# Kernel optimization log

Hardware: AMD Instinct MI355X
Metric: run time of the kernel (lower is better)

The kernel has to match this reference:

```python
import jax, jax.numpy as jnp
import numpy as np

N_NODES = 50000
N_EDGES = 300000
D_IN = 256
D_HID = 256
N_LAYERS = 3
D_OUT = 32
NUM_GRAPHS = 512


def setup_inputs() -> dict:
    key = jax.random.key(0)
    ks = jax.random.split(key, 10)
    x = jax.random.normal(ks[0], (N_NODES, D_IN), dtype=jnp.float32)
    edge_index = jax.random.randint(ks[1], (2, N_EDGES), 0, N_NODES, dtype=jnp.int64)
    batch = jnp.sort(jax.random.randint(ks[2], (N_NODES,), 0, NUM_GRAPHS, dtype=jnp.int64))
    # GraphConv params: out_i = relu(lin_rel(sum_j x_j) + lin_root(x_i)), bias in lin_rel.
    # in_channels == hidden_channels so all nc layers stack into one tensor.
    s = 1.0 / np.sqrt(D_HID)
    W_rel = jax.random.normal(ks[3], (N_LAYERS, D_HID, D_HID), dtype=jnp.float32) * s
    W_root = jax.random.normal(ks[4], (N_LAYERS, D_HID, D_HID), dtype=jnp.float32) * s
    b_conv = jax.random.normal(ks[5], (N_LAYERS, D_HID), dtype=jnp.float32) * s
    W1 = jax.random.normal(ks[6], (D_HID, 4 * D_HID), dtype=jnp.float32) * s
    b1 = jnp.zeros((4 * D_HID,), dtype=jnp.float32)
    W2 = jax.random.normal(ks[7], (4 * D_HID, D_OUT), dtype=jnp.float32) * (1.0 / np.sqrt(4 * D_HID))
    b2 = jnp.zeros((D_OUT,), dtype=jnp.float32)
    return {"x": x, "edge_index": edge_index, "batch": batch,
            "W_rel": W_rel, "W_root": W_root, "b_conv": b_conv,
            "W1": W1, "b1": b1, "W2": W2, "b2": b2,
            "num_graphs": NUM_GRAPHS}


def reference(x, edge_index, batch, W_rel, W_root, b_conv, W1, b1, W2, b2, num_graphs):
    src, dst = edge_index[0], edge_index[1]
    n = x.shape[0]
    # stacked GraphConv(aggr='add') layers with ReLU
    for i in range(W_rel.shape[0]):
        aggr = jax.ops.segment_sum(x[src], dst, num_segments=n)  # [N, d] gather+scatter-add
        x = jax.nn.relu(aggr @ W_rel[i] + x @ W_root[i] + b_conv[i])
    # global_add_pool over graph ids
    pooled = jax.ops.segment_sum(x, batch, num_segments=num_graphs)  # [G, d]
    h = jax.nn.relu(pooled @ W1 + b1)
    return jax.nn.sigmoid(h @ W2 + b2)
```

## Files before the change

kernel.cpp:

```cpp
#include <hip/hip_runtime.h>
#include <math.h>

#define NNODES 50000
#define MPAD   50048
#define D      256
#define K2     512
#define NEDGES 300000
#define NGRAPH 512
#define NLAYERS 3

#define SCB    256
#define NSCB   ((NNODES + SCB - 1) / SCB)

typedef __bf16 bf16x8 __attribute__((ext_vector_type(8)));
typedef float  f32x4  __attribute__((ext_vector_type(4)));

__device__ __forceinline__ ushort f2bf(float f) {
    unsigned u = __float_as_uint(f);
    unsigned r = (u + 0x7FFFu + ((u >> 16) & 1u)) >> 16;
    return (ushort)r;
}
__device__ __forceinline__ float bf2f(ushort b) {
    return __uint_as_float(((unsigned)b) << 16);
}

__device__ __forceinline__ void stage16(const ushort* g, ushort* l) {
    __builtin_amdgcn_global_load_lds(
        (const __attribute__((address_space(1))) unsigned*)g,
        (__attribute__((address_space(3))) unsigned*)l, 16, 0, 0);
}

__global__ __launch_bounds__(256)
void hist_kernel(const int* __restrict__ dst, int* __restrict__ deg, int nE) {
    int e = blockIdx.x * 256 + threadIdx.x;
    if (e < nE) atomicAdd(&deg[dst[e]], 1);
}

__global__ __launch_bounds__(SCB)
void scan_part_kernel(const int* __restrict__ deg, int* __restrict__ bsum) {
    __shared__ int red[SCB];
    int t = threadIdx.x;
    int i = blockIdx.x * SCB + t;
    red[t] = (i < NNODES) ? deg[i] : 0;
    __syncthreads();
#pragma unroll
    for (int off = SCB / 2; off > 0; off >>= 1) {
        if (t < off) red[t] += red[t + off];
        __syncthreads();
    }
    if (t == 0) bsum[blockIdx.x] = red[0];
}

__global__ __launch_bounds__(256)
void scan_bsum_kernel(const int* __restrict__ bsum, int* __restrict__ boff) {
    __shared__ int p[256];
    int t = threadIdx.x;
    p[t] = (t < NSCB) ? bsum[t] : 0;
    __syncthreads();
    for (int off = 1; off < 256; off <<= 1) {
        int v = (t >= off) ? p[t - off] : 0;
        __syncthreads();
        p[t] += v;
        __syncthreads();
    }
    if (t < NSCB) boff[t] = (t == 0) ? 0 : p[t - 1];
}

__global__ __launch_bounds__(SCB)
void scan_final_kernel(const int* __restrict__ deg, const int* __restrict__ boff,
                       int* __restrict__ row_start, int* __restrict__ cursor) {
    __shared__ int p[SCB];
    int t = threadIdx.x;
    int i = blockIdx.x * SCB + t;
    int v = (i < NNODES) ? deg[i] : 0;
    p[t] = v;
    __syncthreads();
    for (int off = 1; off < SCB; off <<= 1) {
        int u = (t >= off) ? p[t - off] : 0;
        __syncthreads();
        p[t] += u;
        __syncthreads();
    }
    int excl = boff[blockIdx.x] + p[t] - v;
    if (i < NNODES) {
        row_start[i] = excl;
        cursor[i] = excl;
    }
    if (blockIdx.x == 0 && t == 0) row_start[NNODES] = NEDGES;
}

__global__ __launch_bounds__(256)
void fill_kernel(const int* __restrict__ src, const int* __restrict__ dst,
                 int* __restrict__ cursor, int* __restrict__ e_src, int nE) {
    int e = blockIdx.x * 256 + threadIdx.x;
    if (e < nE) {
        int pos = atomicAdd(&cursor[dst[e]], 1);
        e_src[pos] = src[e];
    }
}

__global__ __launch_bounds__(256)
void gstart_kernel(const int* __restrict__ batch, int* __restrict__ gstart) {
    int g = blockIdx.x * 256 + threadIdx.x;
    if (g > NGRAPH) return;
    if (g == NGRAPH) { gstart[g] = NNODES; return; }
    int lo = 0, hi = NNODES;
    while (lo < hi) { int mid = (lo + hi) >> 1; if (batch[mid] < g) lo = mid + 1; else hi = mid; }
    gstart[g] = lo;
}

__global__ __launch_bounds__(256)
void prep_w_kernel(const float* __restrict__ W_rel, const float* __restrict__ W_root,
                   ushort* __restrict__ Wh, ushort* __restrict__ Wl) {
    int i = blockIdx.x * 256 + threadIdx.x;
    if (i >= NLAYERS * D * K2) return;
    int L = i / (D * K2);
    int rem = i % (D * K2);
    int n = rem / K2;
    int k = rem % K2;
    float v = (k < D) ? W_rel[(size_t)L * D * D + (size_t)k * D + n]
                      : W_root[(size_t)L * D * D + (size_t)(k - D) * D + n];
    ushort hi = f2bf(v);
    float  lo = v - bf2f(hi);
    Wh[i] = hi;
    Wl[i] = f2bf(lo);
}

__global__ __launch_bounds__(256)
void cvt_x_kernel(const float* __restrict__ x, ushort* __restrict__ xh,
                  ushort* __restrict__ xl) {
    size_t base = ((size_t)blockIdx.x * 256 + threadIdx.x) * 8;
    if (base >= (size_t)MPAD * D) return;
    ushort h[8], l[8];
    if (base < (size_t)NNODES * D) {
        float4 v0 = *reinterpret_cast<const float4*>(x + base);
        float4 v1 = *reinterpret_cast<const float4*>(x + base + 4);
        float vv[8] = {v0.x, v0.y, v0.z, v0.w, v1.x, v1.y, v1.z, v1.w};
#pragma unroll
        for (int j = 0; j < 8; ++j) {
            h[j] = f2bf(vv[j]);
            l[j] = f2bf(vv[j] - bf2f(h[j]));
        }
    } else {
#pragma unroll
        for (int j = 0; j < 8; ++j) { h[j] = 0; l[j] = 0; }
    }
    *reinterpret_cast<uint4*>(xh + base) = *reinterpret_cast<uint4*>(h);
    *reinterpret_cast<uint4*>(xl + base) = *reinterpret_cast<uint4*>(l);
}

__global__ __launch_bounds__(256)
void gather_hl_kernel(const ushort* __restrict__ ph, const ushort* __restrict__ pl,
                      const int* __restrict__ row_start, const int* __restrict__ e_src,
                      ushort* __restrict__ gh, ushort* __restrict__ gl) {
    int t = threadIdx.x;
    int n = blockIdx.x * 4 + (t >> 6);
    if (n >= NNODES) return;
    int lane = t & 63;
    int beg = row_start[n], end = row_start[n + 1];
    float a0 = 0.f, a1 = 0.f, a2 = 0.f, a3 = 0.f;
    int j = beg;
    for (; j + 4 <= end; j += 4) {
        int s0 = e_src[j], s1 = e_src[j + 1], s2 = e_src[j + 2], s3 = e_src[j + 3];
        ushort4 h0 = *reinterpret_cast<const ushort4*>(ph + (size_t)s0 * D + lane * 4);
        ushort4 l0 = *reinterpret_cast<const ushort4*>(pl + (size_t)s0 * D + lane * 4);
        ushort4 h1 = *reinterpret_cast<const ushort4*>(ph + (size_t)s1 * D + lane * 4);
        ushort4 l1 = *reinterpret_cast<const ushort4*>(pl + (size_t)s1 * D + lane * 4);
        ushort4 h2 = *reinterpret_cast<const ushort4*>(ph + (size_t)s2 * D + lane * 4);
        ushort4 l2 = *reinterpret_cast<const ushort4*>(pl + (size_t)s2 * D + lane * 4);
        ushort4 h3 = *reinterpret_cast<const ushort4*>(ph + (size_t)s3 * D + lane * 4);
        ushort4 l3 = *reinterpret_cast<const ushort4*>(pl + (size_t)s3 * D + lane * 4);
        a0 += (bf2f(h0.x) + bf2f(l0.x)) + (bf2f(h1.x) + bf2f(l1.x)) +
              (bf2f(h2.x) + bf2f(l2.x)) + (bf2f(h3.x) + bf2f(l3.x));
        a1 += (bf2f(h0.y) + bf2f(l0.y)) + (bf2f(h1.y) + bf2f(l1.y)) +
              (bf2f(h2.y) + bf2f(l2.y)) + (bf2f(h3.y) + bf2f(l3.y));
        a2 += (bf2f(h0.z) + bf2f(l0.z)) + (bf2f(h1.z) + bf2f(l1.z)) +
              (bf2f(h2.z) + bf2f(l2.z)) + (bf2f(h3.z) + bf2f(l3.z));
        a3 += (bf2f(h0.w) + bf2f(l0.w)) + (bf2f(h1.w) + bf2f(l1.w)) +
              (bf2f(h2.w) + bf2f(l2.w)) + (bf2f(h3.w) + bf2f(l3.w));
    }
    for (; j < end; ++j) {
        int s = e_src[j];
        ushort4 h = *reinterpret_cast<const ushort4*>(ph + (size_t)s * D + lane * 4);
        ushort4 l = *reinterpret_cast<const ushort4*>(pl + (size_t)s * D + lane * 4);
        a0 += bf2f(h.x) + bf2f(l.x);
        a1 += bf2f(h.y) + bf2f(l.y);
        a2 += bf2f(h.z) + bf2f(l.z);
        a3 += bf2f(h.w) + bf2f(l.w);
    }
    ushort4 oh, ol;
    oh.x = f2bf(a0); ol.x = f2bf(a0 - bf2f(oh.x));
    oh.y = f2bf(a1); ol.y = f2bf(a1 - bf2f(oh.y));
    oh.z = f2bf(a2); ol.z = f2bf(a2 - bf2f(oh.z));
    oh.w = f2bf(a3); ol.w = f2bf(a3 - bf2f(oh.w));
    *reinterpret_cast<ushort4*>(gh + (size_t)n * D + lane * 4) = oh;
    *reinterpret_cast<ushort4*>(gl + (size_t)n * D + lane * 4) = ol;
}

#define GBM 128
#define GBN 128
#define GBK 32

__global__ __launch_bounds__(256)
void gemm_hl_kernel(const ushort* __restrict__ Gh, const ushort* __restrict__ Gl,
                    const ushort* __restrict__ Xh, const ushort* __restrict__ Xl,
                    const ushort* __restrict__ Wh, const ushort* __restrict__ Wl,
                    const float* __restrict__ bias,
                    ushort* __restrict__ outh, ushort* __restrict__ outl) {
    __shared__ ushort AhS[GBM * GBK];
    __shared__ ushort AlS[GBM * GBK];
    __shared__ ushort BhS[GBN * GBK];
    __shared__ ushort BlS[GBN * GBK];

    int t = threadIdx.x;
    int wid = t >> 6, lane = t & 63;
    int m0 = blockIdx.x * GBM;
    int n0 = blockIdx.y * GBN;
    int wr = wid >> 1, wc = wid & 1;

    f32x4 acc[4][4];
#pragma unroll
    for (int m = 0; m < 4; ++m)
#pragma unroll
        for (int n = 0; n < 4; ++n)
            acc[m][n] = (f32x4){0.f, 0.f, 0.f, 0.f};

    for (int k0 = 0; k0 < K2; k0 += GBK) {
        const ushort* ah = (k0 < D) ? Gh : Xh;
        const ushort* al = (k0 < D) ? Gl : Xl;
        int kk = k0 & (D - 1);

#pragma unroll
        for (int op = 0; op < 2; ++op) {
            int idx = op * 256 + wid * 64 + lane;
            int row = idx >> 2, sub = idx & 3;
            int kh = ((row >> 1) & 3) ^ sub;
            size_t ldso = (size_t)(op * 256 + wid * 64) * 8;
            stage16(ah + (size_t)(m0 + row) * D + kk + kh * 8, AhS + ldso);
            stage16(al + (size_t)(m0 + row) * D + kk + kh * 8, AlS + ldso);
            stage16(Wh + (size_t)(n0 + row) * K2 + k0 + kh * 8, BhS + ldso);
            stage16(Wl + (size_t)(n0 + row) * K2 + k0 + kh * 8, BlS + ldso);
        }
        __syncthreads();

        bf16x8 fah[4], fal[4], fbh[4], fbl[4];
        int half = lane >> 4;
#pragma unroll
        for (int m = 0; m < 4; ++m) {
            int row = wr * 64 + m * 16 + (lane & 15);
            int off = row * GBK + ((((row >> 1) & 3) ^ half) * 8);
            fah[m] = *reinterpret_cast<const bf16x8*>(&AhS[off]);
            fal[m] = *reinterpret_cast<const bf16x8*>(&AlS[off]);
        }
#pragma unroll
        for (int n = 0; n < 4; ++n) {
            int row = wc * 64 + n * 16 + (lane & 15);
            int off = row * GBK + ((((row >> 1) & 3) ^ half) * 8);
            fbh[n] = *reinterpret_cast<const bf16x8*>(&BhS[off]);
            fbl[n] = *reinterpret_cast<const bf16x8*>(&BlS[off]);
        }
#pragma unroll
        for (int m = 0; m < 4; ++m)
#pragma unroll
            for (int n = 0; n < 4; ++n) {
                acc[m][n] = __builtin_amdgcn_mfma_f32_16x16x32_bf16(fah[m], fbh[n], acc[m][n], 0, 0, 0);
                acc[m][n] = __builtin_amdgcn_mfma_f32_16x16x32_bf16(fah[m], fbl[n], acc[m][n], 0, 0, 0);
                acc[m][n] = __builtin_amdgcn_mfma_f32_16x16x32_bf16(fal[m], fbh[n], acc[m][n], 0, 0, 0);
            }
        __syncthreads();
    }

    int half = lane >> 4;
#pragma unroll
    for (int n = 0; n < 4; ++n) {
        int col = n0 + wc * 64 + n * 16 + (lane & 15);
        float bv = bias[col];
#pragma unroll
        for (int m = 0; m < 4; ++m) {
            int rbase = m0 + wr * 64 + m * 16 + half * 4;
#pragma unroll
            for (int j = 0; j < 4; ++j) {
                int r = rbase + j;
                if (r < NNODES) {
                    float v = fmaxf(acc[m][n][j] + bv, 0.f);
                    ushort hv = f2bf(v);
                    outh[(size_t)r * D + col] = hv;
                    outl[(size_t)r * D + col] = f2bf(v - bf2f(hv));
                }
            }
        }
    }
}

__global__ __launch_bounds__(256)
void pool_seg_kernel(const ushort* __restrict__ ph, const ushort* __restrict__ pl,
                     const int* __restrict__ gstart, float* __restrict__ pooled) {
    __shared__ float red[4][D];
    int g = blockIdx.x;
    int t = threadIdx.x, wid = t >> 6, lane = t & 63;
    int beg = gstart[g], end = gstart[g + 1];
    float a0 = 0.f, a1 = 0.f, a2 = 0.f, a3 = 0.f;
    for (int r = beg + wid; r < end; r += 4) {
        ushort4 h = *reinterpret_cast<const ushort4*>(ph + (size_t)r * D + lane * 4);
        ushort4 l = *reinterpret_cast<const ushort4*>(pl + (size_t)r * D + lane * 4);
        a0 += bf2f(h.x) + bf2f(l.x);
        a1 += bf2f(h.y) + bf2f(l.y);
        a2 += bf2f(h.z) + bf2f(l.z);
        a3 += bf2f(h.w) + bf2f(l.w);
    }
    red[wid][lane * 4 + 0] = a0;
    red[wid][lane * 4 + 1] = a1;
    red[wid][lane * 4 + 2] = a2;
    red[wid][lane * 4 + 3] = a3;
    __syncthreads();
    float s = red[0][t] + red[1][t] + red[2][t] + red[3][t];
    pooled[(size_t)g * D + t] = s;
}

__global__ __launch_bounds__(256)
void mlp1_kernel(const float* __restrict__ pooled, const float* __restrict__ W1,
                 const float* __restrict__ b1, float* __restrict__ h) {
    __shared__ float p[D];
    int g = blockIdx.x, t = threadIdx.x;
    p[t] = pooled[(size_t)g * D + t];
    __syncthreads();
    float4 acc = make_float4(0.f, 0.f, 0.f, 0.f);
    for (int k = 0; k < D; ++k) {
        float4 w = *reinterpret_cast<const float4*>(W1 + (size_t)k * 1024 + t * 4);
        float pv = p[k];
        acc.x += pv * w.x; acc.y += pv * w.y; acc.z += pv * w.z; acc.w += pv * w.w;
    }
    float4 b = *reinterpret_cast<const float4*>(b1 + t * 4);
    acc.x = fmaxf(acc.x + b.x, 0.f);
    acc.y = fmaxf(acc.y + b.y, 0.f);
    acc.z = fmaxf(acc.z + b.z, 0.f);
    acc.w = fmaxf(acc.w + b.w, 0.f);
    *reinterpret_cast<float4*>(h + (size_t)g * 1024 + t * 4) = acc;
}

__global__ __launch_bounds__(256)
void mlp2_kernel(const float* __restrict__ h, const float* __restrict__ W2,
                 const float* __restrict__ b2, float* __restrict__ out) {
    __shared__ float red[8][32];
    int g = blockIdx.x, t = threadIdx.x;
    int c = t & 31, kc = t >> 5;
    float s = 0.f;
    const float* hr = h + (size_t)g * 1024;
    for (int k = kc * 128; k < kc * 128 + 128; ++k)
        s += hr[k] * W2[(size_t)k * 32 + c];
    red[kc][c] = s;
    __syncthreads();
    if (t < 32) {
        float v = b2[t];
#pragma unroll
        for (int i = 0; i < 8; ++i) v += red[i][t];
        out[(size_t)g * 32 + t] = 1.f / (1.f + expf(-v));
    }
}

extern "C" void kernel_launch(void* const* d_in, const int* in_sizes, int n_in,
                              void* d_out, int out_size, void* d_ws, size_t ws_size,
                              hipStream_t stream) {
    const float* x      = (const float*)d_in[0];
    const int*   ei     = (const int*)d_in[1];
    const int*   batch  = (const int*)d_in[2];
    const float* W_rel  = (const float*)d_in[3];
    const float* W_root = (const float*)d_in[4];
    const float* b_conv = (const float*)d_in[5];
    const float* W1     = (const float*)d_in[6];
    const float* b1     = (const float*)d_in[7];
    const float* W2     = (const float*)d_in[8];
    const float* b2     = (const float*)d_in[9];
    float* outp = (float*)d_out;

    const size_t NF = (size_t)MPAD * D;
    ushort* xh = (ushort*)d_ws;
    ushort* xl = xh + NF;
    ushort* yh = xl + NF;
    ushort* yl = yh + NF;
    ushort* gh = yl + NF;
    ushort* gl = gh + NF;
    ushort* Wh = gl + NF;
    ushort* Wl = Wh + (size_t)NLAYERS * D * K2;
    float* pooled = (float*)(Wl + (size_t)NLAYERS * D * K2);
    float* hbuf   = pooled + (size_t)NGRAPH * D;
    int* deg       = (int*)(hbuf + (size_t)NGRAPH * 1024);
    int* row_start = deg + NNODES;
    int* cursor    = row_start + NNODES + 1;
    int* e_src     = cursor + NNODES;
    int* gstart    = e_src + NEDGES;
    int* bsum      = gstart + NGRAPH + 1;
    int* boff      = bsum + NSCB;

    const int* srcp = ei;
    const int* dstp = ei + NEDGES;

    hipMemsetAsync(deg, 0, NNODES * sizeof(int), stream);
    hist_kernel<<<(NEDGES + 255) / 256, 256, 0, stream>>>(dstp, deg, NEDGES);
    scan_part_kernel<<<NSCB, SCB, 0, stream>>>(deg, bsum);
    scan_bsum_kernel<<<1, 256, 0, stream>>>(bsum, boff);
    scan_final_kernel<<<NSCB, SCB, 0, stream>>>(deg, boff, row_start, cursor);
    fill_kernel<<<(NEDGES + 255) / 256, 256, 0, stream>>>(srcp, dstp, cursor, e_src, NEDGES);
    gstart_kernel<<<3, 256, 0, stream>>>(batch, gstart);

    prep_w_kernel<<<(NLAYERS * D * K2 + 255) / 256, 256, 0, stream>>>(W_rel, W_root, Wh, Wl);
    cvt_x_kernel<<<(int)((NF / 8 + 255) / 256), 256, 0, stream>>>(x, xh, xl);

    int gatherBlocks = (NNODES + 3) / 4;
    dim3 ggrid(MPAD / GBM, D / GBN);

    const ushort* curh = xh; const ushort* curl = xl;
    ushort* nxth = yh;       ushort* nxtl = yl;
    for (int L = 0; L < NLAYERS; ++L) {
        gather_hl_kernel<<<gatherBlocks, 256, 0, stream>>>(curh, curl, row_start, e_src, gh, gl);
        gemm_hl_kernel<<<ggrid, 256, 0, stream>>>(gh, gl, curh, curl,
                                                  Wh + (size_t)L * D * K2,
                                                  Wl + (size_t)L * D * K2,
                                                  b_conv + (size_t)L * D,
                                                  nxth, nxtl);
        const ushort* th = curh; const ushort* tl = curl;
        curh = nxth; curl = nxtl;
        nxth = (ushort*)th; nxtl = (ushort*)tl;
        if (L == 0) { nxth = xh; nxtl = xl; }
    }

    pool_seg_kernel<<<NGRAPH, 256, 0, stream>>>(curh, curl, gstart, pooled);
    mlp1_kernel<<<NGRAPH, 256, 0, stream>>>(pooled, W1, b1, hbuf);
    mlp2_kernel<<<NGRAPH, 256, 0, stream>>>(hbuf, W2, b2, outp);
}
```

Measured before the change: 475.9 us.

## Triple-buffer weight tiles in LDS and load activation fragments directly from global

The GraphConv GEMM now keeps only the weight (B) tiles in shared memory, using a three-stage ring buffer that prefetches two K-steps ahead. Explicit vmcnt waits and a single barrier per step replace the two __syncthreads per iteration. Activation (A) fragments are read straight from global memory into registers per wave, skipping the LDS staging. This aims to overlap weight loads with MFMA work and cut barrier overhead, at the cost of uncoalesced, unshared global reads of A, which is duplicated across the two column-waves.

```diff
diff --git a/kernel.cpp b/kernel.cpp
--- a/kernel.cpp
+++ b/kernel.cpp
@@ -200,6 +200,19 @@
 #define GBM 128
 #define GBN 128
 #define GBK 32
+#define NKS (K2 / GBK)
+
+__device__ __forceinline__ void load_a_frags(const ushort* __restrict__ ph,
+                                             const ushort* __restrict__ pl,
+                                             int m0, int wr, int r, int kq, int kk,
+                                             bf16x8 ah[4], bf16x8 al[4]) {
+#pragma unroll
+    for (int m = 0; m < 4; ++m) {
+        size_t o = (size_t)(m0 + wr * 64 + m * 16 + r) * D + kk + kq * 8;
+        ah[m] = *reinterpret_cast<const bf16x8*>(ph + o);
+        al[m] = *reinterpret_cast<const bf16x8*>(pl + o);
+    }
+}
 
 __global__ __launch_bounds__(256)
 void gemm_hl_kernel(const ushort* __restrict__ Gh, const ushort* __restrict__ Gl,
@@ -207,16 +220,14 @@
                     const ushort* __restrict__ Wh, const ushort* __restrict__ Wl,
                     const float* __restrict__ bias,
                     ushort* __restrict__ outh, ushort* __restrict__ outl) {
-    __shared__ ushort AhS[GBM * GBK];
-    __shared__ ushort AlS[GBM * GBK];
-    __shared__ ushort BhS[GBN * GBK];
-    __shared__ ushort BlS[GBN * GBK];
+    __shared__ ushort B_s[3][2][GBN * GBK];
 
     int t = threadIdx.x;
     int wid = t >> 6, lane = t & 63;
     int m0 = blockIdx.x * GBM;
     int n0 = blockIdx.y * GBN;
     int wr = wid >> 1, wc = wid & 1;
+    int r = lane & 15, kq = lane >> 4;
 
     f32x4 acc[4][4];
 #pragma unroll
@@ -225,67 +236,77 @@
         for (int n = 0; n < 4; ++n)
             acc[m][n] = (f32x4){0.f, 0.f, 0.f, 0.f};
 
-    for (int k0 = 0; k0 < K2; k0 += GBK) {
-        const ushort* ah = (k0 < D) ? Gh : Xh;
-        const ushort* al = (k0 < D) ? Gl : Xl;
+    int idxA = wid * 64 + lane;
+    int idxB = 256 + idxA;
+    int rowA = idxA >> 2, khA = ((rowA >> 1) & 3) ^ (idxA & 3);
+    int rowB = idxB >> 2, khB = ((rowB >> 1) & 3) ^ (idxB & 3);
+    size_t loA = (size_t)idxA * 8;
+    size_t loB = (size_t)idxB * 8;
+
+    stage16(Wh + (size_t)(n0 + rowA) * K2 + 0 + khA * 8, &B_s[0][0][loA]);
+    stage16(Wh + (size_t)(n0 + rowB) * K2 + 0 + khB * 8, &B_s[0][0][loB]);
+    stage16(Wl + (size_t)(n0 + rowA) * K2 + 0 + khA * 8, &B_s[0][1][loA]);
+    stage16(Wl + (size_t)(n0 + rowB) * K2 + 0 + khB * 8, &B_s[0][1][loB]);
+    stage16(Wh + (size_t)(n0 + rowA) * K2 + GBK + khA * 8, &B_s[1][0][loA]);
+    stage16(Wh + (size_t)(n0 + rowB) * K2 + GBK + khB * 8, &B_s[1][0][loB]);
+    stage16(Wl + (size_t)(n0 + rowA) * K2 + GBK + khA * 8, &B_s[1][1][loA]);
+    stage16(Wl + (size_t)(n0 + rowB) * K2 + GBK + khB * 8, &B_s[1][1][loB]);
+
+    for (int ks = 0; ks < NKS; ++ks) {
+        if (ks < NKS - 1) asm volatile("s_waitcnt vmcnt(4)" ::: "memory");
+        else              asm volatile("s_waitcnt vmcnt(0)" ::: "memory");
+        __builtin_amdgcn_s_barrier();
+        __builtin_amdgcn_sched_barrier(0);
+
+        if (ks + 2 < NKS) {
+            int kn = (ks + 2) * GBK;
+            int bn = (ks + 2) % 3;
+            stage16(Wh + (size_t)(n0 + rowA) * K2 + kn + khA * 8, &B_s[bn][0][loA]);
+            stage16(Wh + (size_t)(n0 + rowB) * K2 + kn + khB * 8, &B_s[bn][0][loB]);
+            stage16(Wl + (size_t)(n0 + rowA) * K2 + kn + khA * 8, &B_s[bn][1][loA]);
+            stage16(Wl + (size_t)(n0 + rowB) * K2 + kn + khB * 8, &B_s[bn][1][loB]);
+        }
+
+        int k0 = ks * GBK;
+        const ushort* ph = (k0 < D) ? Gh : Xh;
+        const ushort* pl = (k0 < D) ? Gl : Xl;
         int kk = k0 & (D - 1);
-
-#pragma unroll
-        for (int op = 0; op < 2; ++op) {
-            int idx = op * 256 + wid * 64 + lane;
-            int row = idx >> 2, sub = idx & 3;
-            int kh = ((row >> 1) & 3) ^ sub;
-            size_t ldso = (size_t)(op * 256 + wid * 64) * 8;
-            stage16(ah + (size_t)(m0 + row) * D + kk + kh * 8, AhS + ldso);
-            stage16(al + (size_t)(m0 + row) * D + kk + kh * 8, AlS + ldso);
-            stage16(Wh + (size_t)(n0 + row) * K2 + k0 + kh * 8, BhS + ldso);
-            stage16(Wl + (size_t)(n0 + row) * K2 + k0 + kh * 8, BlS + ldso);
+        bf16x8 ah[4], al[4], bh[4], bl[4];
+        load_a_frags(ph, pl, m0, wr, r, kq, kk, ah, al);
+
+        int cb = ks % 3;
+#pragma unroll
+        for (int n = 0; n < 4; ++n) {
+            int rw = wc * 64 + n * 16 + r;
+            int off = rw * GBK + ((((rw >> 1) & 3) ^ kq) * 8);
+            bh[n] = *reinterpret_cast<const bf16x8*>(&B_s[cb][0][off]);
+            bl[n] = *reinterpret_cast<const bf16x8*>(&B_s[cb][1][off]);
         }
-        __syncthreads();
-
-        bf16x8 fah[4], fal[4], fbh[4], fbl[4];
-        int half = lane >> 4;
+#pragma unroll
+        for (int m = 0; m < 4; ++m)
+#pragma unroll
+            for (int n = 0; n < 4; ++n) {
+                acc[m][n] = __builtin_amdgcn_mfma_f32_16x16x32_bf16(ah[m], bh[n], acc[m][n], 0, 0, 0);
+                acc[m][n] = __builtin_amdgcn_mfma_f32_16x16x32_bf16(ah[m], bl[n], acc[m][n], 0, 0, 0);
+                acc[m][n] = __builtin_amdgcn_mfma_f32_16x16x32_bf16(al[m], bh[n], acc[m][n], 0, 0, 0);
+            }
+    }
+
+#pragma unroll
+    for (int n = 0; n < 4; ++n) {
+        int col = n0 + wc * 64 + n * 16 + r;
+        float bv = bias[col];
 #pragma unroll
         for (int m = 0; m < 4; ++m) {
-            int row = wr * 64 + m * 16 + (lane & 15);
-            int off = row * GBK + ((((row >> 1) & 3) ^ half) * 8);
-            fah[m] = *reinterpret_cast<const bf16x8*>(&AhS[off]);
-            fal[m] = *reinterpret_cast<const bf16x8*>(&AlS[off]);
-        }
-#pragma unroll
-        for (int n = 0; n < 4; ++n) {
-            int row = wc * 64 + n * 16 + (lane & 15);
-            int off = row * GBK + ((((row >> 1) & 3) ^ half) * 8);
-            fbh[n] = *reinterpret_cast<const bf16x8*>(&BhS[off]);
-            fbl[n] = *reinterpret_cast<const bf16x8*>(&BlS[off]);
-        }
-#pragma unroll
-        for (int m = 0; m < 4; ++m)
-#pragma unroll
-            for (int n = 0; n < 4; ++n) {
-                acc[m][n] = __builtin_amdgcn_mfma_f32_16x16x32_bf16(fah[m], fbh[n], acc[m][n], 0, 0, 0);
-                acc[m][n] = __builtin_amdgcn_mfma_f32_16x16x32_bf16(fah[m], fbl[n], acc[m][n], 0, 0, 0);
-                acc[m][n] = __builtin_amdgcn_mfma_f32_16x16x32_bf16(fal[m], fbh[n], acc[m][n], 0, 0, 0);
-            }
-        __syncthreads();
-    }
-
-    int half = lane >> 4;
-#pragma unroll
-    for (int n = 0; n < 4; ++n) {
-        int col = n0 + wc * 64 + n * 16 + (lane & 15);
-        float bv = bias[col];
-#pragma unroll
-        for (int m = 0; m < 4; ++m) {
-            int rbase = m0 + wr * 64 + m * 16 + half * 4;
+            int rbase = m0 + wr * 64 + m * 16 + kq * 4;
 #pragma unroll
             for (int j = 0; j < 4; ++j) {
-                int r = rbase + j;
-                if (r < NNODES) {
+                int rr = rbase + j;
+                if (rr < NNODES) {
                     float v = fmaxf(acc[m][n][j] + bv, 0.f);
                     ushort hv = f2bf(v);
-                    outh[(size_t)r * D + col] = hv;
-                    outl[(size_t)r * D + col] = f2bf(v - bf2f(hv));
+                    outh[(size_t)rr * D + col] = hv;
+                    outl[(size_t)rr * D + col] = f2bf(v - bf2f(hv));
                 }
             }
         }
@@ -300,9 +321,9 @@
     int t = threadIdx.x, wid = t >> 6, lane = t & 63;
     int beg = gstart[g], end = gstart[g + 1];
     float a0 = 0.f, a1 = 0.f, a2 = 0.f, a3 = 0.f;
-    for (int r = beg + wid; r < end; r += 4) {
-        ushort4 h = *reinterpret_cast<const ushort4*>(ph + (size_t)r * D + lane * 4);
-        ushort4 l = *reinterpret_cast<const ushort4*>(pl + (size_t)r * D + lane * 4);
+    for (int rr = beg + wid; rr < end; rr += 4) {
+        ushort4 h = *reinterpret_cast<const ushort4*>(ph + (size_t)rr * D + lane * 4);
+        ushort4 l = *reinterpret_cast<const ushort4*>(pl + (size_t)rr * D + lane * 4);
         a0 += bf2f(h.x) + bf2f(l.x);
         a1 += bf2f(h.y) + bf2f(l.y);
         a2 += bf2f(h.z) + bf2f(l.z);
```

Measured after the change: 566.7 us. 19.1% more time.
